# Optimization experiments

Hardware: AMD Instinct MI355X
Metric: run time of the kernel (lower is better)

Reference implementation:

```python
import jax, jax.numpy as jnp
import numpy as np

IN_F, OUT_F, RANK, ALPHA = 4096, 4096, 8, 32.0

def setup_inputs() -> dict:
    key = jax.random.key(0)
    kx, kw, ka, kb, kbias = jax.random.split(key, 5)
    x = jax.random.normal(kx, (4, 2048, IN_F), dtype=jnp.float32)
    weight = jax.random.normal(kw, (OUT_F, IN_F), dtype=jnp.float32) * 0.02
    a = jax.random.normal(ka, (OUT_F, RANK), dtype=jnp.float32) * 0.02
    b = jax.random.normal(kb, (RANK, IN_F), dtype=jnp.float32) * 0.02  # zeros in init; use randn for nontrivial test
    bias = jax.random.normal(kbias, (OUT_F,), dtype=jnp.float32) * 0.02
    return {"x": x, "weight": weight, "a": a, "b": b, "bias": bias}

def reference(x, weight, a, b, bias):
    # F.linear(x, W, bias) + F.linear(x, a @ b) * alpha / r
    base = jnp.einsum('bsi,oi->bso', x, weight) + bias
    # low-rank path computed in factored form (same math as x @ (a@b).T)
    lora = jnp.einsum('bsr,or->bso', jnp.einsum('bsi,ri->bsr', x, b), a)
    return base + lora * (ALPHA / RANK)
```

## Files before the change

### kernel.cpp

```cpp
#include <hip/hip_runtime.h>
#include <stdint.h>

#define IN_F 4096
#define OUT_F 4096
#define M_TOT 8192
#define LORA_SCALE 4.0f

typedef unsigned short u16;
typedef __attribute__((ext_vector_type(8))) short bf16x8;
typedef __attribute__((ext_vector_type(4))) float f32x4;

__device__ __forceinline__ u16 f2bf(float f) {
  union { float f; unsigned u; } v; v.f = f;
  unsigned r = v.u + 0x7FFFu + ((v.u >> 16) & 1u);
  return (u16)(r >> 16);
}

__device__ __forceinline__ void gload_lds16(const void* g, void* l) {
  __builtin_amdgcn_global_load_lds(
      (const __attribute__((address_space(1))) void*)g,
      (__attribute__((address_space(3))) void*)l, 16, 0, 0);
}

__global__ void prep(const float* __restrict__ X, const float* __restrict__ W,
                     const float* __restrict__ A, const float* __restrict__ B,
                     u16* __restrict__ Xb, u16* __restrict__ Wb) {
  int bid = blockIdx.x;
  if (bid < 16384) {
    size_t base = ((size_t)bid * blockDim.x + threadIdx.x) * 8;
    const f32x4* p = (const f32x4*)(X + base);
    f32x4 v0 = __builtin_nontemporal_load(p);
    f32x4 v1 = __builtin_nontemporal_load(p + 1);
    uint4 pk;
    pk.x = (unsigned)f2bf(v0.x) | ((unsigned)f2bf(v0.y) << 16);
    pk.y = (unsigned)f2bf(v0.z) | ((unsigned)f2bf(v0.w) << 16);
    pk.z = (unsigned)f2bf(v1.x) | ((unsigned)f2bf(v1.y) << 16);
    pk.w = (unsigned)f2bf(v1.z) | ((unsigned)f2bf(v1.w) << 16);
    *(uint4*)(Xb + base) = pk;
  } else {
    int idx = (bid - 16384) * blockDim.x + threadIdx.x;
    int o  = idx >> 10;
    int i0 = (idx & 1023) << 2;
    const f32x4 w = __builtin_nontemporal_load((const f32x4*)(W + (size_t)o * IN_F + i0));
    float a0 = w.x, a1 = w.y, a2 = w.z, a3 = w.w;
#pragma unroll
    for (int r = 0; r < 8; ++r) {
      float ar = A[o * 8 + r] * LORA_SCALE;
      const float4 bv = *(const float4*)(B + (size_t)r * IN_F + i0);
      a0 += ar * bv.x; a1 += ar * bv.y; a2 += ar * bv.z; a3 += ar * bv.w;
    }
    uint2 pk;
    pk.x = (unsigned)f2bf(a0) | ((unsigned)f2bf(a1) << 16);
    pk.y = (unsigned)f2bf(a2) | ((unsigned)f2bf(a3) << 16);
    *(uint2*)(Wb + (size_t)o * IN_F + i0) = pk;
  }
}


#define ABASE(b) ((b) * 32768)
#define BBASE(b) ((b) * 32768 + 16384)

#define STAGE_A(b, h, kt) \
  gload_lds16(aG + (size_t)((h) * 128) * IN_F + (kt), lds + ABASE(b) + ((h) * 128) * 64 + tid * 8)

#define STAGE_B(b, h, kt) \
  gload_lds16(bG + (size_t)((h) * 128) * IN_F + (kt), lds + BBASE(b) + ((h) * 128) * 64 + tid * 8)

#define WAIT2 asm volatile("s_waitcnt vmcnt(2)" ::: "memory")
#define WAIT0 asm volatile("s_waitcnt vmcnt(0)" ::: "memory")

#define MFMA16 __builtin_amdgcn_mfma_f32_16x16x32_bf16

#define KHALF(b, CKX, TAIL_STAGE) do { \
  __builtin_amdgcn_s_barrier(); \
  __builtin_amdgcn_sched_barrier(0); \
  _Pragma("unroll") \
  for (int n = 0; n < 4; ++n) \
    Bf[n] = *(const bf16x8*)(lds + BBASE(b) + (rB + n * 16) * 64 + (CKX)); \
  _Pragma("unroll") \
  for (int m = 0; m < 4; ++m) \
    Af[m] = *(const bf16x8*)(lds + ABASE(b) + (rA + m * 16) * 64 + (CKX)); \
  __builtin_amdgcn_s_setprio(1); \
  _Pragma("unroll") \
  for (int m = 0; m < 4; ++m) \
    _Pragma("unroll") \
    for (int n = 0; n < 4; ++n) \
      acc[m][n] = MFMA16(Af[m], Bf[n], acc[m][n], 0, 0, 0); \
  __builtin_amdgcn_s_setprio(0); \
  TAIL_STAGE; \
} while (0)

__global__ __launch_bounds__(1024, 4) void gemm8(const u16* __restrict__ Xb,
                                                 const u16* __restrict__ Wb,
                                                 const float* __restrict__ bias,
                                                 float* __restrict__ out) {
  extern __shared__ u16 lds[];

  const int tid  = threadIdx.x;
  const int lane = tid & 63;
  const int wid  = tid >> 6;
  const int wr = wid >> 2, wc = wid & 3;
  const int lr = lane & 15, kg = lane >> 4;

  const int bid = blockIdx.x;
  const int swz = (bid & 7) * 64 + (bid >> 3);
  const int mt = swz >> 4, nt = swz & 15;
  const int m0 = mt * 256, n0 = nt * 256;

  const int srow = tid >> 3;
  const int swc  = (tid & 7) ^ (srow & 7);
  const u16* aG = Xb + (size_t)(m0 + srow) * IN_F + swc * 8;
  const u16* bG = Wb + (size_t)(n0 + srow) * IN_F + swc * 8;

  const int rA = wr * 64 + lr;
  const int rB = wc * 64 + lr;
  const int ck0 = ((kg) ^ (lane & 7)) * 8;
  const int ck1 = ((4 + kg) ^ (lane & 7)) * 8;

  f32x4 acc[4][4] = {};
  bf16x8 Af[4], Bf[4];

  STAGE_B(0, 0, 0); STAGE_B(0, 1, 0);
  STAGE_A(0, 0, 0); STAGE_A(0, 1, 0);
  STAGE_B(1, 0, 64); STAGE_B(1, 1, 64);
  WAIT2;

  for (int i = 0; i < 31; ++i) {
    const int kt1 = i * 128 + 64, kt2 = i * 128 + 128, kt3 = i * 128 + 192;
    KHALF(0, ck0, STAGE_A(1, 0, kt1); STAGE_A(1, 1, kt1));
    KHALF(0, ck1, STAGE_B(0, 0, kt2); STAGE_B(0, 1, kt2));
    WAIT2;
    KHALF(1, ck0, STAGE_A(0, 0, kt2); STAGE_A(0, 1, kt2));
    KHALF(1, ck1, STAGE_B(1, 0, kt3); STAGE_B(1, 1, kt3));
    WAIT2;
  }
  KHALF(0, ck0, STAGE_A(1, 0, 4032); STAGE_A(1, 1, 4032));
  KHALF(0, ck1, );
  WAIT0;
  KHALF(1, ck0, );
  KHALF(1, ck1, );

  float bv[4];
#pragma unroll
  for (int n = 0; n < 4; ++n) bv[n] = bias[n0 + wc * 64 + n * 16 + lr];
  const int rbase = m0 + wr * 64 + kg * 4;
#pragma unroll
  for (int m = 0; m < 4; ++m)
#pragma unroll
    for (int n = 0; n < 4; ++n) {
      int col = n0 + wc * 64 + n * 16 + lr;
#pragma unroll
      for (int r = 0; r < 4; ++r)
        __builtin_nontemporal_store(acc[m][n][r] + bv[n],
                                    &out[(size_t)(rbase + m * 16 + r) * OUT_F + col]);
    }
}

__global__ __launch_bounds__(256) void gemm_bias(const u16* __restrict__ Xb,
                                                 const u16* __restrict__ Wb,
                                                 const float* __restrict__ bias,
                                                 float* __restrict__ out) {
  __shared__ __align__(16) u16 ldsA[128 * 64];
  __shared__ __align__(16) u16 ldsB[128 * 64];

  const int tid  = threadIdx.x;
  const int wid  = tid >> 6;
  const int lane = tid & 63;
  const int nt = blockIdx.x & 31;
  const int mt = blockIdx.x >> 5;
  const int m0 = mt * 128, n0 = nt * 128;
  const int wr = wid >> 1, wc = wid & 1;
  const int lr = lane & 15;
  const int kg = lane >> 4;

  const int srow   = wid * 8 + (lane >> 3);
  const int schunk = (lane & 7) ^ (srow & 7);
  const u16* aSrc = Xb + (size_t)(m0 + srow) * IN_F + schunk * 8;
  const u16* bSrc = Wb + (size_t)(n0 + srow) * IN_F + schunk * 8;

  f32x4 acc[4][4] = {};

  for (int kt = 0; kt < IN_F; kt += 64) {
    __syncthreads();
#pragma unroll
    for (int j = 0; j < 4; ++j) {
      gload_lds16(aSrc + (size_t)(j * 32) * IN_F + kt, &ldsA[j * 2048 + wid * 512]);
      gload_lds16(bSrc + (size_t)(j * 32) * IN_F + kt, &ldsB[j * 2048 + wid * 512]);
    }
    __syncthreads();

#pragma unroll
    for (int s = 0; s < 2; ++s) {
      bf16x8 af[4], bfr[4];
#pragma unroll
      for (int m = 0; m < 4; ++m) {
        int r = wr * 64 + m * 16 + lr;
        int c = (s * 4 + kg) ^ (r & 7);
        af[m] = *(const bf16x8*)&ldsA[r * 64 + c * 8];
      }
#pragma unroll
      for (int n = 0; n < 4; ++n) {
        int r = wc * 64 + n * 16 + lr;
        int c = (s * 4 + kg) ^ (r & 7);
        bfr[n] = *(const bf16x8*)&ldsB[r * 64 + c * 8];
      }
#pragma unroll
      for (int m = 0; m < 4; ++m)
#pragma unroll
        for (int n = 0; n < 4; ++n)
          acc[m][n] = __builtin_amdgcn_mfma_f32_16x16x32_bf16(af[m], bfr[n], acc[m][n], 0, 0, 0);
    }
  }

  float bv[4];
#pragma unroll
  for (int n = 0; n < 4; ++n) bv[n] = bias[n0 + wc * 64 + n * 16 + lr];
  const int rbase = m0 + wr * 64 + kg * 4;
#pragma unroll
  for (int m = 0; m < 4; ++m)
#pragma unroll
    for (int n = 0; n < 4; ++n) {
      int col = n0 + wc * 64 + n * 16 + lr;
#pragma unroll
      for (int r = 0; r < 4; ++r)
        out[(size_t)(rbase + m * 16 + r) * OUT_F + col] = acc[m][n][r] + bv[n];
    }
}

__global__ void lora_t(const float* __restrict__ x, const float* __restrict__ B,
                       float* __restrict__ t) {
  int m = blockIdx.x;
  int tid = threadIdx.x, lane = tid & 63;
  float p[8] = {0, 0, 0, 0, 0, 0, 0, 0};
  for (int k = tid; k < IN_F; k += 256) {
    float xv = x[(size_t)m * IN_F + k];
#pragma unroll
    for (int r = 0; r < 8; ++r) p[r] += xv * B[r * IN_F + k];
  }
#pragma unroll
  for (int r = 0; r < 8; ++r) {
    float v = p[r];
    for (int off = 32; off; off >>= 1) v += __shfl_down(v, off);
    if (lane == 0) atomicAdd(&t[m * 8 + r], v);
  }
}

__global__ void fb_gemm(const float* __restrict__ x, const float* __restrict__ W,
                        const float* __restrict__ A, const float* __restrict__ bias,
                        const float* __restrict__ t, float* __restrict__ out) {
  __shared__ float sx[64][17];
  __shared__ float sw[64][17];
  int tx = threadIdx.x, ty = threadIdx.y;
  int tid = ty * 16 + tx;
  int m0 = blockIdx.y * 64, n0 = blockIdx.x * 64;
  float acc[4][4] = {};
  for (int kt = 0; kt < IN_F; kt += 16) {
    __syncthreads();
#pragma unroll
    for (int q = 0; q < 4; ++q) {
      int idx = q * 256 + tid;
      int r = idx >> 4, c = idx & 15;
      sx[r][c] = x[(size_t)(m0 + r) * IN_F + kt + c];
      sw[r][c] = W[(size_t)(n0 + r) * IN_F + kt + c];
    }
    __syncthreads();
#pragma unroll
    for (int k = 0; k < 16; ++k) {
      float xv[4], wv[4];
#pragma unroll
      for (int i = 0; i < 4; ++i) xv[i] = sx[ty * 4 + i][k];
#pragma unroll
      for (int j = 0; j < 4; ++j) wv[j] = sw[tx * 4 + j][k];
#pragma unroll
      for (int i = 0; i < 4; ++i)
#pragma unroll
        for (int j = 0; j < 4; ++j) acc[i][j] += xv[i] * wv[j];
    }
  }
#pragma unroll
  for (int i = 0; i < 4; ++i) {
    int m = m0 + ty * 4 + i;
    float tv[8];
#pragma unroll
    for (int r = 0; r < 8; ++r) tv[r] = t[m * 8 + r];
#pragma unroll
    for (int j = 0; j < 4; ++j) {
      int o = n0 + tx * 4 + j;
      float lora = 0.f;
#pragma unroll
      for (int r = 0; r < 8; ++r) lora += tv[r] * A[o * 8 + r];
      out[(size_t)m * OUT_F + o] = acc[i][j] + bias[o] + LORA_SCALE * lora;
    }
  }
}

extern "C" void kernel_launch(void* const* d_in, const int* in_sizes, int n_in,
                              void* d_out, int out_size, void* d_ws, size_t ws_size,
                              hipStream_t stream) {
  const float* x    = (const float*)d_in[0];
  const float* W    = (const float*)d_in[1];
  const float* A    = (const float*)d_in[2];
  const float* B    = (const float*)d_in[3];
  const float* bias = (const float*)d_in[4];
  float* out = (float*)d_out;

  const size_t xb_elems = (size_t)M_TOT * IN_F;
  const size_t wb_elems = (size_t)OUT_F * IN_F;
  const size_t need = (xb_elems + wb_elems) * sizeof(u16);

  if (ws_size >= need) {
    u16* Xb = (u16*)d_ws;
    u16* Wb = Xb + xb_elems;
    prep<<<32768, 256, 0, stream>>>(x, W, A, B, Xb, Wb);

    hipError_t e = hipFuncSetAttribute((const void*)gemm8,
                                       hipFuncAttributeMaxDynamicSharedMemorySize,
                                       131072);
    bool used8 = false;
    if (e == hipSuccess) {
      gemm8<<<512, 1024, 131072, stream>>>(Xb, Wb, bias, out);
      used8 = (hipGetLastError() == hipSuccess);
    }
    if (!used8) {
      gemm_bias<<<(M_TOT / 128) * (OUT_F / 128), 256, 0, stream>>>(Xb, Wb, bias, out);
    }
  } else {
    float* t = (float*)d_ws;
    (void)hipMemsetAsync(t, 0, (size_t)M_TOT * 8 * sizeof(float), stream);
    lora_t<<<M_TOT, 256, 0, stream>>>(x, B, t);
    fb_gemm<<<dim3(OUT_F / 64, M_TOT / 64), dim3(16, 16), 0, stream>>>(x, W, A, bias, t, out);
  }
}
```

Before: 294.0 us.

## Fuse fp32-to-bf16 conversion of X into the GEMM main loop

Drops the separate pass that converted the activations to bf16. The GEMM now loads fp32 X tiles into registers, converts them to bf16 and writes them to LDS itself, while W stays on the async global-to-LDS path. This removes one full read and write of X through memory, but each block now fetches twice as many bytes of X per tile. The pipeline also waits on all outstanding vector loads (vmcnt(0)) before each LDS write, which reduces load/compute overlap. The bf16 X conversion kernel is kept only for the fallback GEMM.

```diff
diff --git a/kernel.cpp b/kernel.cpp
--- a/kernel.cpp
+++ b/kernel.cpp
@@ -22,56 +22,72 @@
       (__attribute__((address_space(3))) void*)l, 16, 0, 0);
 }
 
-__global__ void prep(const float* __restrict__ X, const float* __restrict__ W,
-                     const float* __restrict__ A, const float* __restrict__ B,
-                     u16* __restrict__ Xb, u16* __restrict__ Wb) {
-  int bid = blockIdx.x;
-  if (bid < 16384) {
-    size_t base = ((size_t)bid * blockDim.x + threadIdx.x) * 8;
-    const f32x4* p = (const f32x4*)(X + base);
-    f32x4 v0 = __builtin_nontemporal_load(p);
-    f32x4 v1 = __builtin_nontemporal_load(p + 1);
-    uint4 pk;
-    pk.x = (unsigned)f2bf(v0.x) | ((unsigned)f2bf(v0.y) << 16);
-    pk.y = (unsigned)f2bf(v0.z) | ((unsigned)f2bf(v0.w) << 16);
-    pk.z = (unsigned)f2bf(v1.x) | ((unsigned)f2bf(v1.y) << 16);
-    pk.w = (unsigned)f2bf(v1.z) | ((unsigned)f2bf(v1.w) << 16);
-    *(uint4*)(Xb + base) = pk;
-  } else {
-    int idx = (bid - 16384) * blockDim.x + threadIdx.x;
-    int o  = idx >> 10;
-    int i0 = (idx & 1023) << 2;
-    const f32x4 w = __builtin_nontemporal_load((const f32x4*)(W + (size_t)o * IN_F + i0));
-    float a0 = w.x, a1 = w.y, a2 = w.z, a3 = w.w;
-#pragma unroll
-    for (int r = 0; r < 8; ++r) {
-      float ar = A[o * 8 + r] * LORA_SCALE;
-      const float4 bv = *(const float4*)(B + (size_t)r * IN_F + i0);
-      a0 += ar * bv.x; a1 += ar * bv.y; a2 += ar * bv.z; a3 += ar * bv.w;
-    }
-    uint2 pk;
-    pk.x = (unsigned)f2bf(a0) | ((unsigned)f2bf(a1) << 16);
-    pk.y = (unsigned)f2bf(a2) | ((unsigned)f2bf(a3) << 16);
-    *(uint2*)(Wb + (size_t)o * IN_F + i0) = pk;
-  }
+__global__ void prep_w(const float* __restrict__ W, const float* __restrict__ A,
+                       const float* __restrict__ B, u16* __restrict__ Wb) {
+  int idx = blockIdx.x * blockDim.x + threadIdx.x;
+  int o  = idx >> 10;
+  int i0 = (idx & 1023) << 2;
+  const f32x4 w = __builtin_nontemporal_load((const f32x4*)(W + (size_t)o * IN_F + i0));
+  float a0 = w.x, a1 = w.y, a2 = w.z, a3 = w.w;
+#pragma unroll
+  for (int r = 0; r < 8; ++r) {
+    float ar = A[o * 8 + r] * LORA_SCALE;
+    const float4 bv = *(const float4*)(B + (size_t)r * IN_F + i0);
+    a0 += ar * bv.x; a1 += ar * bv.y; a2 += ar * bv.z; a3 += ar * bv.w;
+  }
+  uint2 pk;
+  pk.x = (unsigned)f2bf(a0) | ((unsigned)f2bf(a1) << 16);
+  pk.y = (unsigned)f2bf(a2) | ((unsigned)f2bf(a3) << 16);
+  *(uint2*)(Wb + (size_t)o * IN_F + i0) = pk;
+}
+
+__global__ void convert_x(const float* __restrict__ X, u16* __restrict__ Xb) {
+  size_t base = ((size_t)blockIdx.x * blockDim.x + threadIdx.x) * 8;
+  const f32x4* p = (const f32x4*)(X + base);
+  f32x4 v0 = __builtin_nontemporal_load(p);
+  f32x4 v1 = __builtin_nontemporal_load(p + 1);
+  uint4 pk;
+  pk.x = (unsigned)f2bf(v0.x) | ((unsigned)f2bf(v0.y) << 16);
+  pk.y = (unsigned)f2bf(v0.z) | ((unsigned)f2bf(v0.w) << 16);
+  pk.z = (unsigned)f2bf(v1.x) | ((unsigned)f2bf(v1.y) << 16);
+  pk.w = (unsigned)f2bf(v1.z) | ((unsigned)f2bf(v1.w) << 16);
+  *(uint4*)(Xb + base) = pk;
 }
 
 
 #define ABASE(b) ((b) * 32768)
 #define BBASE(b) ((b) * 32768 + 16384)
 
-#define STAGE_A(b, h, kt) \
-  gload_lds16(aG + (size_t)((h) * 128) * IN_F + (kt), lds + ABASE(b) + ((h) * 128) * 64 + tid * 8)
-
 #define STAGE_B(b, h, kt) \
   gload_lds16(bG + (size_t)((h) * 128) * IN_F + (kt), lds + BBASE(b) + ((h) * 128) * 64 + tid * 8)
 
-#define WAIT2 asm volatile("s_waitcnt vmcnt(2)" ::: "memory")
+#define LOAD_A(kt) do { \
+  av00 = *(const f32x4*)(xG + (size_t)(kt)); \
+  av01 = *(const f32x4*)(xG + (size_t)(kt) + 4); \
+  av10 = *(const f32x4*)(xG + (size_t)128 * IN_F + (kt)); \
+  av11 = *(const f32x4*)(xG + (size_t)128 * IN_F + (kt) + 4); \
+} while (0)
+
+#define CVT_WRITE_A(b) do { \
+  uint4 p0, p1; \
+  p0.x = (unsigned)f2bf(av00.x) | ((unsigned)f2bf(av00.y) << 16); \
+  p0.y = (unsigned)f2bf(av00.z) | ((unsigned)f2bf(av00.w) << 16); \
+  p0.z = (unsigned)f2bf(av01.x) | ((unsigned)f2bf(av01.y) << 16); \
+  p0.w = (unsigned)f2bf(av01.z) | ((unsigned)f2bf(av01.w) << 16); \
+  p1.x = (unsigned)f2bf(av10.x) | ((unsigned)f2bf(av10.y) << 16); \
+  p1.y = (unsigned)f2bf(av10.z) | ((unsigned)f2bf(av10.w) << 16); \
+  p1.z = (unsigned)f2bf(av11.x) | ((unsigned)f2bf(av11.y) << 16); \
+  p1.w = (unsigned)f2bf(av11.z) | ((unsigned)f2bf(av11.w) << 16); \
+  *(uint4*)(lds + ABASE(b) + tid * 8) = p0; \
+  *(uint4*)(lds + ABASE(b) + 8192 + tid * 8) = p1; \
+} while (0)
+
 #define WAIT0 asm volatile("s_waitcnt vmcnt(0)" ::: "memory")
+#define LGKM0 asm volatile("s_waitcnt lgkmcnt(0)" ::: "memory")
 
 #define MFMA16 __builtin_amdgcn_mfma_f32_16x16x32_bf16
 
-#define KHALF(b, CKX, TAIL_STAGE) do { \
+#define KHALF(b, CKX, MID_STMT, TAIL_STMT) do { \
   __builtin_amdgcn_s_barrier(); \
   __builtin_amdgcn_sched_barrier(0); \
   _Pragma("unroll") \
@@ -80,6 +96,7 @@
   _Pragma("unroll") \
   for (int m = 0; m < 4; ++m) \
     Af[m] = *(const bf16x8*)(lds + ABASE(b) + (rA + m * 16) * 64 + (CKX)); \
+  MID_STMT; \
   __builtin_amdgcn_s_setprio(1); \
   _Pragma("unroll") \
   for (int m = 0; m < 4; ++m) \
@@ -87,10 +104,10 @@
     for (int n = 0; n < 4; ++n) \
       acc[m][n] = MFMA16(Af[m], Bf[n], acc[m][n], 0, 0, 0); \
   __builtin_amdgcn_s_setprio(0); \
-  TAIL_STAGE; \
+  TAIL_STMT; \
 } while (0)
 
-__global__ __launch_bounds__(1024, 4) void gemm8(const u16* __restrict__ Xb,
+__global__ __launch_bounds__(1024, 4) void gemm8(const float* __restrict__ X,
                                                  const u16* __restrict__ Wb,
                                                  const float* __restrict__ bias,
                                                  float* __restrict__ out) {
@@ -109,8 +126,8 @@
 
   const int srow = tid >> 3;
   const int swc  = (tid & 7) ^ (srow & 7);
-  const u16* aG = Xb + (size_t)(m0 + srow) * IN_F + swc * 8;
-  const u16* bG = Wb + (size_t)(n0 + srow) * IN_F + swc * 8;
+  const float* xG = X + (size_t)(m0 + srow) * IN_F + swc * 8;
+  const u16*   bG = Wb + (size_t)(n0 + srow) * IN_F + swc * 8;
 
   const int rA = wr * 64 + lr;
   const int rB = wc * 64 + lr;
@@ -119,26 +136,28 @@
 
   f32x4 acc[4][4] = {};
   bf16x8 Af[4], Bf[4];
+  f32x4 av00, av01, av10, av11;
 
   STAGE_B(0, 0, 0); STAGE_B(0, 1, 0);
-  STAGE_A(0, 0, 0); STAGE_A(0, 1, 0);
+  LOAD_A(0);
+  WAIT0;
+  CVT_WRITE_A(0);
   STAGE_B(1, 0, 64); STAGE_B(1, 1, 64);
-  WAIT2;
+  LGKM0;
 
   for (int i = 0; i < 31; ++i) {
     const int kt1 = i * 128 + 64, kt2 = i * 128 + 128, kt3 = i * 128 + 192;
-    KHALF(0, ck0, STAGE_A(1, 0, kt1); STAGE_A(1, 1, kt1));
-    KHALF(0, ck1, STAGE_B(0, 0, kt2); STAGE_B(0, 1, kt2));
-    WAIT2;
-    KHALF(1, ck0, STAGE_A(0, 0, kt2); STAGE_A(0, 1, kt2));
-    KHALF(1, ck1, STAGE_B(1, 0, kt3); STAGE_B(1, 1, kt3));
-    WAIT2;
-  }
-  KHALF(0, ck0, STAGE_A(1, 0, 4032); STAGE_A(1, 1, 4032));
-  KHALF(0, ck1, );
-  WAIT0;
-  KHALF(1, ck0, );
-  KHALF(1, ck1, );
+    KHALF(0, ck0, LOAD_A(kt1), );
+    KHALF(0, ck1, ,
+          WAIT0; CVT_WRITE_A(1); STAGE_B(0, 0, kt2); STAGE_B(0, 1, kt2); LGKM0);
+    KHALF(1, ck0, LOAD_A(kt2), );
+    KHALF(1, ck1, ,
+          WAIT0; CVT_WRITE_A(0); STAGE_B(1, 0, kt3); STAGE_B(1, 1, kt3); LGKM0);
+  }
+  KHALF(0, ck0, LOAD_A(4032), );
+  KHALF(0, ck1, , WAIT0; CVT_WRITE_A(1); LGKM0);
+  KHALF(1, ck0, , );
+  KHALF(1, ck1, , );
 
   float bv[4];
 #pragma unroll
@@ -306,22 +325,22 @@
 
   const size_t xb_elems = (size_t)M_TOT * IN_F;
   const size_t wb_elems = (size_t)OUT_F * IN_F;
-  const size_t need = (xb_elems + wb_elems) * sizeof(u16);
-
-  if (ws_size >= need) {
+
+  if (ws_size >= (xb_elems + wb_elems) * sizeof(u16)) {
     u16* Xb = (u16*)d_ws;
     u16* Wb = Xb + xb_elems;
-    prep<<<32768, 256, 0, stream>>>(x, W, A, B, Xb, Wb);
+    prep_w<<<16384, 256, 0, stream>>>(W, A, B, Wb);
 
     hipError_t e = hipFuncSetAttribute((const void*)gemm8,
                                        hipFuncAttributeMaxDynamicSharedMemorySize,
                                        131072);
     bool used8 = false;
     if (e == hipSuccess) {
-      gemm8<<<512, 1024, 131072, stream>>>(Xb, Wb, bias, out);
+      gemm8<<<512, 1024, 131072, stream>>>(x, Wb, bias, out);
       used8 = (hipGetLastError() == hipSuccess);
     }
     if (!used8) {
+      convert_x<<<(M_TOT * IN_F / 8) / 256, 256, 0, stream>>>(x, Xb);
       gemm_bias<<<(M_TOT / 128) * (OUT_F / 128), 256, 0, stream>>>(Xb, Wb, bias, out);
     }
   } else {
```

New measurement: 698.5 us. 2.38x slower.

## Triple-buffer B tiles and issue prefetch before MFMAs in gemm8

Applied to the files above, without the earlier changes.

Reworks the gemm8 K-loop pipeline. Each 64-wide K tile now has two A buffers and three rotating B buffers, and LDS grows to 160 KB. The loads for the next A and B tiles are issued right after the first fragment reads, before the MFMAs, instead of after them. This gives global-to-LDS loads more time in flight and halves the number of barriers per K step. The cost is more LDS use and a more complex rotation schedule, which could introduce race or correctness risks.

```diff
diff --git a/kernel.cpp b/kernel.cpp
--- a/kernel.cpp
+++ b/kernel.cpp
@@ -57,29 +57,34 @@
 }
 
 
-#define ABASE(b) ((b) * 32768)
-#define BBASE(b) ((b) * 32768 + 16384)
-
-#define STAGE_A(b, h, kt) \
-  gload_lds16(aG + (size_t)((h) * 128) * IN_F + (kt), lds + ABASE(b) + ((h) * 128) * 64 + tid * 8)
-
-#define STAGE_B(b, h, kt) \
-  gload_lds16(bG + (size_t)((h) * 128) * IN_F + (kt), lds + BBASE(b) + ((h) * 128) * 64 + tid * 8)
+#define ABASE(ab) ((ab) * 16384)
+#define BBASE(j)  (32768 + (j) * 16384)
+
+#define STAGE_A2(ab, kt) do { \
+  gload_lds16(aG + (size_t)(kt),                lds + ABASE(ab) + tid * 8); \
+  gload_lds16(aG + (size_t)128 * IN_F + (kt),   lds + ABASE(ab) + 8192 + tid * 8); \
+} while (0)
+
+#define STAGE_B2(j, kt) do { \
+  gload_lds16(bG + (size_t)(kt),                lds + BBASE(j) + tid * 8); \
+  gload_lds16(bG + (size_t)128 * IN_F + (kt),   lds + BBASE(j) + 8192 + tid * 8); \
+} while (0)
 
 #define WAIT2 asm volatile("s_waitcnt vmcnt(2)" ::: "memory")
 #define WAIT0 asm volatile("s_waitcnt vmcnt(0)" ::: "memory")
 
 #define MFMA16 __builtin_amdgcn_mfma_f32_16x16x32_bf16
 
-#define KHALF(b, CKX, TAIL_STAGE) do { \
+#define KTILE(ab, bj, STAGE_STMT, WAIT_STMT) do { \
   __builtin_amdgcn_s_barrier(); \
   __builtin_amdgcn_sched_barrier(0); \
   _Pragma("unroll") \
   for (int n = 0; n < 4; ++n) \
-    Bf[n] = *(const bf16x8*)(lds + BBASE(b) + (rB + n * 16) * 64 + (CKX)); \
+    Bf[n] = *(const bf16x8*)(lds + BBASE(bj) + (rB + n * 16) * 64 + ck0); \
   _Pragma("unroll") \
   for (int m = 0; m < 4; ++m) \
-    Af[m] = *(const bf16x8*)(lds + ABASE(b) + (rA + m * 16) * 64 + (CKX)); \
+    Af[m] = *(const bf16x8*)(lds + ABASE(ab) + (rA + m * 16) * 64 + ck0); \
+  STAGE_STMT; \
   __builtin_amdgcn_s_setprio(1); \
   _Pragma("unroll") \
   for (int m = 0; m < 4; ++m) \
@@ -87,7 +92,20 @@
     for (int n = 0; n < 4; ++n) \
       acc[m][n] = MFMA16(Af[m], Bf[n], acc[m][n], 0, 0, 0); \
   __builtin_amdgcn_s_setprio(0); \
-  TAIL_STAGE; \
+  _Pragma("unroll") \
+  for (int n = 0; n < 4; ++n) \
+    Bf[n] = *(const bf16x8*)(lds + BBASE(bj) + (rB + n * 16) * 64 + ck1); \
+  _Pragma("unroll") \
+  for (int m = 0; m < 4; ++m) \
+    Af[m] = *(const bf16x8*)(lds + ABASE(ab) + (rA + m * 16) * 64 + ck1); \
+  __builtin_amdgcn_s_setprio(1); \
+  _Pragma("unroll") \
+  for (int m = 0; m < 4; ++m) \
+    _Pragma("unroll") \
+    for (int n = 0; n < 4; ++n) \
+      acc[m][n] = MFMA16(Af[m], Bf[n], acc[m][n], 0, 0, 0); \
+  __builtin_amdgcn_s_setprio(0); \
+  WAIT_STMT; \
 } while (0)
 
 __global__ __launch_bounds__(1024, 4) void gemm8(const u16* __restrict__ Xb,
@@ -120,25 +138,24 @@
   f32x4 acc[4][4] = {};
   bf16x8 Af[4], Bf[4];
 
-  STAGE_B(0, 0, 0); STAGE_B(0, 1, 0);
-  STAGE_A(0, 0, 0); STAGE_A(0, 1, 0);
-  STAGE_B(1, 0, 64); STAGE_B(1, 1, 64);
+  STAGE_B2(0, 0);
+  STAGE_A2(0, 0);
+  STAGE_B2(1, 64);
   WAIT2;
 
-  for (int i = 0; i < 31; ++i) {
-    const int kt1 = i * 128 + 64, kt2 = i * 128 + 128, kt3 = i * 128 + 192;
-    KHALF(0, ck0, STAGE_A(1, 0, kt1); STAGE_A(1, 1, kt1));
-    KHALF(0, ck1, STAGE_B(0, 0, kt2); STAGE_B(0, 1, kt2));
-    WAIT2;
-    KHALF(1, ck0, STAGE_A(0, 0, kt2); STAGE_A(0, 1, kt2));
-    KHALF(1, ck1, STAGE_B(1, 0, kt3); STAGE_B(1, 1, kt3));
-    WAIT2;
-  }
-  KHALF(0, ck0, STAGE_A(1, 0, 4032); STAGE_A(1, 1, 4032));
-  KHALF(0, ck1, );
-  WAIT0;
-  KHALF(1, ck0, );
-  KHALF(1, ck1, );
+  for (int g = 0; g < 10; ++g) {
+    const int k0 = g * 384;
+    KTILE(0, 0, STAGE_A2(1, k0 + 64);  STAGE_B2(2, k0 + 128), WAIT2);
+    KTILE(1, 1, STAGE_A2(0, k0 + 128); STAGE_B2(0, k0 + 192), WAIT2);
+    KTILE(0, 2, STAGE_A2(1, k0 + 192); STAGE_B2(1, k0 + 256), WAIT2);
+    KTILE(1, 0, STAGE_A2(0, k0 + 256); STAGE_B2(2, k0 + 320), WAIT2);
+    KTILE(0, 1, STAGE_A2(1, k0 + 320); STAGE_B2(0, k0 + 384), WAIT2);
+    KTILE(1, 2, STAGE_A2(0, k0 + 384); STAGE_B2(1, k0 + 448), WAIT2);
+  }
+  KTILE(0, 0, STAGE_A2(1, 3904); STAGE_B2(2, 3968), WAIT2);
+  KTILE(1, 1, STAGE_A2(0, 3968); STAGE_B2(0, 4032), WAIT2);
+  KTILE(0, 2, STAGE_A2(1, 4032), WAIT0);
+  KTILE(1, 0, , );
 
   float bv[4];
 #pragma unroll
@@ -306,19 +323,18 @@
 
   const size_t xb_elems = (size_t)M_TOT * IN_F;
   const size_t wb_elems = (size_t)OUT_F * IN_F;
-  const size_t need = (xb_elems + wb_elems) * sizeof(u16);
-
-  if (ws_size >= need) {
+
+  if (ws_size >= (xb_elems + wb_elems) * sizeof(u16)) {
     u16* Xb = (u16*)d_ws;
     u16* Wb = Xb + xb_elems;
     prep<<<32768, 256, 0, stream>>>(x, W, A, B, Xb, Wb);
 
     hipError_t e = hipFuncSetAttribute((const void*)gemm8,
                                        hipFuncAttributeMaxDynamicSharedMemorySize,
-                                       131072);
+                                       163840);
     bool used8 = false;
     if (e == hipSuccess) {
-      gemm8<<<512, 1024, 131072, stream>>>(Xb, Wb, bias, out);
+      gemm8<<<512, 1024, 163840, stream>>>(Xb, Wb, bias, out);
       used8 = (hipGetLastError() == hipSuccess);
     }
     if (!used8) {
```

Result: no change. 296.4 us (+0.8%).
